# Performance work log

Measured on AMD Instinct MI355X. Metric: run time of the kernel, lower is better.

## Reference

```python
import jax, jax.numpy as jnp
import numpy as np

N_GENE = 4762
N_CELL = 847


def _graph_conv(x_src, src, dst, n_src, n_dst, W, b):
    """DGL GraphConv with norm='both': D_src^{-1/2} A D_dst^{-1/2} X W + b."""
    ones_e = jnp.ones(src.shape, jnp.float32)
    deg_out = jax.ops.segment_sum(ones_e, src, num_segments=n_src)
    norm_src = jnp.clip(deg_out, 1.0, None) ** -0.5
    feat = x_src * norm_src[:, None]            # [n_src, d]
    msg = feat[src]                              # gather  [E, d]
    agg = jax.ops.segment_sum(msg, dst, num_segments=n_dst)  # scatter-add [n_dst, d]
    deg_in = jax.ops.segment_sum(ones_e, dst, num_segments=n_dst)
    norm_dst = jnp.clip(deg_in, 1.0, None) ** -0.5
    return (agg * norm_dst[:, None]) @ W + b


def setup_inputs() -> dict:
    key = jax.random.key(0)
    ks = jax.random.split(key, 12)
    E = 200000
    d = 256
    inp = {
        "gene_emb": jax.random.normal(ks[0], (N_GENE, d), jnp.float32),
        "cell_emb": jax.random.normal(ks[1], (N_CELL, d), jnp.float32),
        "W_g2c": jax.random.normal(ks[2], (d, d), jnp.float32) * (1.0 / np.sqrt(d)),
        "b_g2c": jnp.zeros((d,), jnp.float32),
        "W_c2g": jax.random.normal(ks[3], (d, d), jnp.float32) * (1.0 / np.sqrt(d)),
        "b_c2g": jnp.zeros((d,), jnp.float32),
        "Wp": jax.random.normal(ks[4], (2 * d, 1), jnp.float32) * (1.0 / np.sqrt(2 * d)),
        "bp": jnp.zeros((1,), jnp.float32),
        "g2c_src": jax.random.randint(ks[5], (E,), 0, N_GENE, jnp.int32),
        "g2c_dst": jax.random.randint(ks[6], (E,), 0, N_CELL, jnp.int32),
        "c2g_src": jax.random.randint(ks[7], (E,), 0, N_CELL, jnp.int32),
        "c2g_dst": jax.random.randint(ks[8], (E,), 0, N_GENE, jnp.int32),
        "dec_src": jax.random.randint(ks[9], (E,), 0, N_GENE, jnp.int32),
        "dec_dst": jax.random.randint(ks[10], (E,), 0, N_CELL, jnp.int32),
    }
    return inp


def reference(gene_emb, cell_emb, W_g2c, b_g2c, W_c2g, b_c2g, Wp, bp,
              g2c_src, g2c_dst, c2g_src, c2g_dst, dec_src, dec_dst):
    # HeteroGraphConv (aggregate='sum'): each dst type receives from one relation here.
    h_cell = _graph_conv(gene_emb, g2c_src, g2c_dst, N_GENE, N_CELL, W_g2c, b_g2c)
    h_gene = _graph_conv(cell_emb, c2g_src, c2g_dst, N_CELL, N_GENE, W_c2g, b_c2g)
    h_gene = jax.nn.relu(h_gene)
    h_cell = jax.nn.relu(h_cell)
    # HeteroMLPPredictor: concat(src_h, dst_h) @ Wp + bp on dec_graph edges.
    x = jnp.concatenate([h_gene[dec_src], h_cell[dec_dst]], axis=1)  # [E_dec, 512]
    score = x @ Wp + bp                                               # [E_dec, 1]
    return (score, h_gene, h_cell)
```

## Files before the change

kernel.cpp:

```cpp
#include <hip/hip_runtime.h>

#define N_GENE 4762
#define N_CELL 847
#define NEDGE  200000
#define D      256
#define NPART  64

typedef __attribute__((ext_vector_type(8))) short short8;
typedef __attribute__((ext_vector_type(8))) unsigned short ushort8v;
typedef __attribute__((ext_vector_type(4))) float f32x4;

#define S_G_OUT 0
#define S_C_IN  (S_G_OUT + N_GENE)
#define S_C_OUT (S_C_IN + N_CELL)
#define S_G_IN  (S_C_OUT + N_CELL)
#define NBINS   (S_G_IN + N_GENE)

#define ALIGN8(x) (((x) + 7) & ~7)

#define A_DEG      0
#define A_NRM      (A_DEG + NBINS)
#define A_OFFS_C   (A_NRM + NBINS)
#define A_OFFS_G   (A_OFFS_C + N_CELL + 1)
#define A_SORT_C   ALIGN8(A_OFFS_G + N_GENE + 1)
#define A_SORT_G   (A_SORT_C + 2 * NEDGE)
#define A_PART     (A_SORT_G + 2 * NEDGE)
#define A_SG       (A_PART + NPART * NBINS)
#define A_SC       (A_SG + N_GENE)
#define A_GENE_BF  ALIGN8(A_SC + N_CELL)
#define A_CELL_BF  ALIGN8(A_GENE_BF + N_GENE * D / 2)
#define A_WT1_BF   ALIGN8(A_CELL_BF + N_CELL * D / 2)
#define A_WT2_BF   ALIGN8(A_WT1_BF + D * D / 2)
#define A_AGGC_BF  ALIGN8(A_WT2_BF + D * D / 2)
#define A_AGGG_BF  ALIGN8(A_AGGC_BF + N_CELL * D / 2)

__device__ __forceinline__ unsigned short f2bf(float f) {
    unsigned u = __float_as_uint(f);
    u = (u + 0x7FFFu + ((u >> 16) & 1u)) >> 16;
    return (unsigned short)u;
}
__device__ __forceinline__ float bf2f(unsigned short b) {
    return __uint_as_float(((unsigned)b) << 16);
}

__global__ __launch_bounds__(1024) void k_pre(
        const int* __restrict__ g2c_src, const int* __restrict__ g2c_dst,
        const int* __restrict__ c2g_src, const int* __restrict__ c2g_dst,
        const float* __restrict__ gene_emb, const float* __restrict__ cell_emb,
        const float* __restrict__ W_g2c, const float* __restrict__ W_c2g,
        int* __restrict__ partial,
        unsigned short* __restrict__ gene_bf, unsigned short* __restrict__ cell_bf,
        unsigned short* __restrict__ wt1, unsigned short* __restrict__ wt2) {
    __shared__ int sh[NBINS];
    int B = blockIdx.x, T = threadIdx.x;
    if (B < NPART) {
        for (int j = T; j < NBINS; j += 1024) sh[j] = 0;
        __syncthreads();
        const int chunk = (NEDGE + NPART - 1) / NPART;
        int e0 = B * chunk, e1 = min(NEDGE, e0 + chunk);
        for (int e = e0 + T; e < e1; e += 1024) {
            atomicAdd(&sh[S_G_OUT + g2c_src[e]], 1);
            atomicAdd(&sh[S_C_IN  + g2c_dst[e]], 1);
            atomicAdd(&sh[S_C_OUT + c2g_src[e]], 1);
            atomicAdd(&sh[S_G_IN  + c2g_dst[e]], 1);
        }
        __syncthreads();
        int* pp = partial + B * NBINS;
        for (int j = T; j < NBINS; j += 1024) pp[j] = sh[j];
    } else {
        const int NG = N_GENE * D, NC = N_CELL * D, NW = D * D;
        const int total = NG + NC + 2 * NW;
        for (int i = (B - NPART) * 1024 + T; i < total; i += NPART * 1024) {
            if (i < NG) {
                gene_bf[i] = f2bf(gene_emb[i]);
            } else if (i < NG + NC) {
                int j = i - NG;
                cell_bf[j] = f2bf(cell_emb[j]);
            } else if (i < NG + NC + NW) {
                int j = i - NG - NC;
                wt1[j] = f2bf(W_g2c[(j & 255) * D + (j >> 8)]);
            } else {
                int j = i - NG - NC - NW;
                wt2[j] = f2bf(W_c2g[(j & 255) * D + (j >> 8)]);
            }
        }
    }
}

__global__ void k_reduce(int* __restrict__ partial, int* __restrict__ deg,
                         float* __restrict__ nrm) {
    int j = blockIdx.x * blockDim.x + threadIdx.x;
    if (j < NBINS) {
        int s = 0;
        #pragma unroll
        for (int b0 = 0; b0 < NPART; b0 += 32) {
            int t[32];
            #pragma unroll
            for (int u = 0; u < 32; u++) t[u] = partial[(b0 + u) * NBINS + j];
            #pragma unroll
            for (int u = 0; u < 32; u++) { partial[(b0 + u) * NBINS + j] = s; s += t[u]; }
        }
        deg[j] = s;
        nrm[j] = rsqrtf(fmaxf((float)s, 1.0f));
    }
}

__global__ __launch_bounds__(1024) void k_scatter(
        const int* __restrict__ g2c_src, const int* __restrict__ g2c_dst,
        const int* __restrict__ c2g_src, const int* __restrict__ c2g_dst,
        const int* __restrict__ deg, const int* __restrict__ partial,
        const float* __restrict__ nrm,
        int* __restrict__ offsC, int* __restrict__ offsG,
        int2* __restrict__ sortC, int2* __restrict__ sortG) {
    __shared__ int soffs[N_GENE + 1];
    __shared__ int scur[N_GENE];
    __shared__ int wsum[16];
    int T = threadIdx.x, blk = blockIdx.x, dir = blockIdx.y;
    const int* src  = dir ? c2g_src : g2c_src;
    const int* dst  = dir ? c2g_dst : g2c_dst;
    const int* dgs  = dir ? deg + S_G_IN : deg + S_C_IN;
    const float* nsv = dir ? nrm + S_C_OUT : nrm + S_G_OUT;
    int seg         = dir ? S_G_IN : S_C_IN;
    int nb          = dir ? N_GENE : N_CELL;
    int* goffs      = dir ? offsG : offsC;
    int2* sorted    = dir ? sortG : sortC;
    int per = (nb + 1023) >> 10;
    int i0 = T * per, i1 = min(nb, i0 + per);
    int loc[5];
    int s = 0;
    for (int i = i0; i < i1; i++) { loc[i - i0] = s; s += dgs[i]; }
    int lane = T & 63, w = T >> 6;
    int t = s;
    #pragma unroll
    for (int off = 1; off < 64; off <<= 1) {
        int u = __shfl_up(t, off);
        if (lane >= off) t += u;
    }
    if (lane == 63) wsum[w] = t;
    __syncthreads();
    if (w == 0 && lane < 16) {
        int x = wsum[lane];
        #pragma unroll
        for (int off = 1; off < 16; off <<= 1) {
            int u = __shfl_up(x, off);
            if (lane >= off) x += u;
        }
        wsum[lane] = x;
    }
    __syncthreads();
    int wbase = w ? wsum[w - 1] : 0;
    int excl = wbase + t - s;
    for (int i = i0; i < i1; i++) soffs[i] = excl + loc[i - i0];
    if (T == 1023) soffs[nb] = excl + s;
    __syncthreads();
    if (blk == 0)
        for (int j = T; j <= nb; j += 1024) goffs[j] = soffs[j];
    const int* basep = partial + blk * NBINS + seg;
    for (int j = T; j < nb; j += 1024) scur[j] = soffs[j] + basep[j];
    __syncthreads();
    const int chunk = (NEDGE + NPART - 1) / NPART;
    int e0 = blk * chunk, e1 = min(NEDGE, e0 + chunk);
    for (int e = e0 + T; e < e1; e += 1024) {
        int d = dst[e], sv = src[e];
        float nv = nsv[sv];
        int pos = atomicAdd(&scur[d], 1);
        sorted[pos] = make_int2(sv, __float_as_int(nv));
    }
}

__global__ __launch_bounds__(256) void k_agg(
        const unsigned short* __restrict__ gene_bf,
        const unsigned short* __restrict__ cell_bf,
        const int2* __restrict__ sortC, const int2* __restrict__ sortG,
        const int* __restrict__ offsC, const int* __restrict__ offsG,
        const float* __restrict__ nrm,
        unsigned short* __restrict__ aggC, unsigned short* __restrict__ aggG) {
    __shared__ int   sidx[4][64];
    __shared__ float snrm[4][64];
    __shared__ float pacc[4][256];
    int w = threadIdx.x >> 6, lane = threadIdx.x & 63;
    int half = lane >> 5, li = lane & 31;
    int B = blockIdx.x;
    bool isCell = B < N_CELL;

    int e0, e1;
    const unsigned short* emb;
    const int2* sorted;
    int node;
    if (isCell) {
        node = B;
        int f0 = offsC[node], f1 = offsC[node + 1];
        int ne = f1 - f0, nw = (ne + 3) >> 2;
        e0 = f0 + w * nw; e1 = min(f1, e0 + nw);
        emb = gene_bf; sorted = sortC;
    } else {
        node = (B - N_CELL) * 4 + w;
        if (node >= N_GENE) return;
        e0 = offsG[node]; e1 = offsG[node + 1];
        emb = cell_bf; sorted = sortG;
    }

    float acc[8];
    #pragma unroll
    for (int c = 0; c < 8; c++) acc[c] = 0.f;

    for (int base = e0; base < e1; base += 64) {
        int n = min(64, e1 - base);
        if (lane < n) {
            int2 pr = sorted[base + lane];
            sidx[w][lane] = pr.x;
            snrm[w][lane] = __int_as_float(pr.y);
        }
        int i = 0;
        for (; 2 * i + 8 <= n; i += 4) {
            int j0 = 2 * i + half, j1 = 2 * i + 2 + half;
            int j2 = 2 * i + 4 + half, j3 = 2 * i + 6 + half;
            ushort8v v0 = *(const ushort8v*)&emb[sidx[w][j0] * D + li * 8];
            ushort8v v1 = *(const ushort8v*)&emb[sidx[w][j1] * D + li * 8];
            ushort8v v2 = *(const ushort8v*)&emb[sidx[w][j2] * D + li * 8];
            ushort8v v3 = *(const ushort8v*)&emb[sidx[w][j3] * D + li * 8];
            float n0 = snrm[w][j0], n1 = snrm[w][j1];
            float n2 = snrm[w][j2], n3 = snrm[w][j3];
            #pragma unroll
            for (int c = 0; c < 8; c++)
                acc[c] += bf2f(v0[c]) * n0 + bf2f(v1[c]) * n1 +
                          bf2f(v2[c]) * n2 + bf2f(v3[c]) * n3;
        }
        int npair = (n + 1) >> 1;
        for (; i < npair; i++) {
            int jj = 2 * i + half;
            bool ok = jj < n;
            int idx = ok ? sidx[w][jj] : sidx[w][0];
            float nv = ok ? snrm[w][jj] : 0.f;
            ushort8v v = *(const ushort8v*)&emb[idx * D + li * 8];
            #pragma unroll
            for (int c = 0; c < 8; c++) acc[c] += bf2f(v[c]) * nv;
        }
    }
    #pragma unroll
    for (int c = 0; c < 8; c++) acc[c] += __shfl_xor(acc[c], 32);

    if (isCell) {
        if (half == 0) {
            #pragma unroll
            for (int c = 0; c < 8; c++) pacc[w][li * 8 + c] = acc[c];
        }
        __syncthreads();
        int T = threadIdx.x;
        float s2 = pacc[0][T] + pacc[1][T] + pacc[2][T] + pacc[3][T];
        aggC[node * D + T] = f2bf(s2 * nrm[S_C_IN + node]);
    } else {
        if (half == 0) {
            float ndv = nrm[S_G_IN + node];
            ushort8v o;
            #pragma unroll
            for (int c = 0; c < 8; c++) o[c] = f2bf(acc[c] * ndv);
            *(ushort8v*)&aggG[node * D + li * 8] = o;
        }
    }
}

__global__ __launch_bounds__(256) void k_gemm2(
        const unsigned short* __restrict__ aggC, const unsigned short* __restrict__ aggG,
        const unsigned short* __restrict__ wt1, const unsigned short* __restrict__ wt2,
        const float* __restrict__ b_g2c, const float* __restrict__ b_c2g,
        const float* __restrict__ Wp,
        float* __restrict__ hC, float* __restrict__ hG,
        float* __restrict__ sg, float* __restrict__ sc) {
    const int CT = (N_CELL + 15) / 16;
    const int GT = (N_GENE + 15) / 16;
    int wid = blockIdx.x * 4 + (threadIdx.x >> 6);
    if (wid >= CT + GT) return;
    bool isCell = wid < CT;
    int tile = isCell ? wid : wid - CT;
    int m0 = tile * 16;
    int M = isCell ? N_CELL : N_GENE;
    const unsigned short* A  = isCell ? aggC : aggG;
    const unsigned short* Wt = isCell ? wt1 : wt2;
    const float* bias = isCell ? b_g2c : b_c2g;
    const float* wp   = isCell ? Wp + D : Wp;
    float* H  = isCell ? hC : hG;
    float* sv = isCell ? sc : sg;
    int lane = threadIdx.x & 63;
    int l15 = lane & 15, quad = lane >> 4;
    int arow = m0 + l15;
    if (arow >= M) arow = M - 1;
    f32x4 acc[16];
    #pragma unroll
    for (int t = 0; t < 16; t++) acc[t] = (f32x4){0.f, 0.f, 0.f, 0.f};
    #pragma unroll
    for (int k0 = 0; k0 < D; k0 += 32) {
        short8 a = *(const short8*)&A[arow * D + k0 + quad * 8];
        #pragma unroll
        for (int t = 0; t < 16; t++) {
            short8 b = *(const short8*)&Wt[(t * 16 + l15) * D + k0 + quad * 8];
            acc[t] = __builtin_amdgcn_mfma_f32_16x16x32_bf16(a, b, acc[t], 0, 0, 0);
        }
    }
    float dot[4] = {0.f, 0.f, 0.f, 0.f};
    #pragma unroll
    for (int t = 0; t < 16; t++) {
        int col = t * 16 + l15;
        float bv = bias[col], wv = wp[col];
        #pragma unroll
        for (int r = 0; r < 4; r++) {
            int row = m0 + quad * 4 + r;
            float h = fmaxf(acc[t][r] + bv, 0.f);
            if (row < M) H[row * D + col] = h;
            dot[r] += h * wv;
        }
    }
    #pragma unroll
    for (int off = 1; off < 16; off <<= 1) {
        #pragma unroll
        for (int r = 0; r < 4; r++) dot[r] += __shfl_xor(dot[r], off);
    }
    if (l15 == 0) {
        #pragma unroll
        for (int r = 0; r < 4; r++) {
            int row = m0 + quad * 4 + r;
            if (row < M) sv[row] = dot[r];
        }
    }
}

__global__ void k_score(const int* __restrict__ dsrc, const int* __restrict__ ddst,
                        const float* __restrict__ sg, const float* __restrict__ sc,
                        const float* __restrict__ bp, float* __restrict__ out) {
    int i = blockIdx.x * blockDim.x + threadIdx.x;
    if (i < NEDGE) out[i] = sg[dsrc[i]] + sc[ddst[i]] + bp[0];
}

extern "C" void kernel_launch(void* const* d_in, const int* in_sizes, int n_in,
                              void* d_out, int out_size, void* d_ws, size_t ws_size,
                              hipStream_t stream) {
    const float* gene_emb = (const float*)d_in[0];
    const float* cell_emb = (const float*)d_in[1];
    const float* W_g2c    = (const float*)d_in[2];
    const float* b_g2c    = (const float*)d_in[3];
    const float* W_c2g    = (const float*)d_in[4];
    const float* b_c2g    = (const float*)d_in[5];
    const float* Wp       = (const float*)d_in[6];
    const float* bp       = (const float*)d_in[7];
    const int* g2c_src = (const int*)d_in[8];
    const int* g2c_dst = (const int*)d_in[9];
    const int* c2g_src = (const int*)d_in[10];
    const int* c2g_dst = (const int*)d_in[11];
    const int* dec_src = (const int*)d_in[12];
    const int* dec_dst = (const int*)d_in[13];

    int*   wsi = (int*)d_ws;
    float* wsf = (float*)d_ws;
    unsigned short* gene_bf = (unsigned short*)(wsi + A_GENE_BF);
    unsigned short* cell_bf = (unsigned short*)(wsi + A_CELL_BF);
    unsigned short* wt1     = (unsigned short*)(wsi + A_WT1_BF);
    unsigned short* wt2     = (unsigned short*)(wsi + A_WT2_BF);
    unsigned short* aggC    = (unsigned short*)(wsi + A_AGGC_BF);
    unsigned short* aggG    = (unsigned short*)(wsi + A_AGGG_BF);
    int2* sortC = (int2*)(wsi + A_SORT_C);
    int2* sortG = (int2*)(wsi + A_SORT_G);

    float* out = (float*)d_out;
    float* out_score = out;
    float* out_hgene = out + NEDGE;
    float* out_hcell = out + NEDGE + N_GENE * D;

    k_pre<<<2 * NPART, 1024, 0, stream>>>(g2c_src, g2c_dst, c2g_src, c2g_dst,
                                          gene_emb, cell_emb, W_g2c, W_c2g,
                                          wsi + A_PART, gene_bf, cell_bf, wt1, wt2);
    k_reduce<<<(NBINS + 255) / 256, 256, 0, stream>>>(wsi + A_PART, wsi + A_DEG,
                                                      wsf + A_NRM);
    {
        dim3 grid(NPART, 2);
        k_scatter<<<grid, 1024, 0, stream>>>(g2c_src, g2c_dst, c2g_src, c2g_dst,
                                             wsi + A_DEG, wsi + A_PART, wsf + A_NRM,
                                             wsi + A_OFFS_C, wsi + A_OFFS_G,
                                             sortC, sortG);
    }
    k_agg<<<N_CELL + (N_GENE + 3) / 4, 256, 0, stream>>>(
        gene_bf, cell_bf, sortC, sortG, wsi + A_OFFS_C, wsi + A_OFFS_G,
        wsf + A_NRM, aggC, aggG);
    {
        const int CT = (N_CELL + 15) / 16, GT = (N_GENE + 15) / 16;
        k_gemm2<<<(CT + GT + 3) / 4, 256, 0, stream>>>(aggC, aggG, wt1, wt2,
                                                       b_g2c, b_c2g, Wp,
                                                       out_hcell, out_hgene,
                                                       wsf + A_SG, wsf + A_SC);
    }
    k_score<<<(NEDGE + 255) / 256, 256, 0, stream>>>(dec_src, dec_dst,
                                                     wsf + A_SG, wsf + A_SC, bp, out_score);
}
```

Measured before the change: 158.9 us.

## Fuse front and back kernel chains with software grid barriers; deepen aggregation unroll

```diff
diff --git a/kernel.cpp b/kernel.cpp
--- a/kernel.cpp
+++ b/kernel.cpp
@@ -33,6 +33,7 @@
 #define A_WT2_BF   ALIGN8(A_WT1_BF + D * D / 2)
 #define A_AGGC_BF  ALIGN8(A_WT2_BF + D * D / 2)
 #define A_AGGG_BF  ALIGN8(A_AGGC_BF + N_CELL * D / 2)
+#define A_CTR      ALIGN8(A_AGGG_BF + N_GENE * D / 2)
 
 __device__ __forceinline__ unsigned short f2bf(float f) {
     unsigned u = __float_as_uint(f);
@@ -43,16 +44,37 @@
     return __uint_as_float(((unsigned)b) << 16);
 }
 
-__global__ __launch_bounds__(1024) void k_pre(
+__device__ __forceinline__ void gbar(int* ctr, int target) {
+    __syncthreads();
+    if (threadIdx.x == 0) {
+        __hip_atomic_fetch_add(ctr, 1, __ATOMIC_ACQ_REL, __HIP_MEMORY_SCOPE_AGENT);
+        long long t0 = (long long)__builtin_amdgcn_s_memrealtime();
+        while (__hip_atomic_load(ctr, __ATOMIC_ACQUIRE, __HIP_MEMORY_SCOPE_AGENT) < target) {
+            __builtin_amdgcn_s_sleep(2);
+            if ((long long)__builtin_amdgcn_s_memrealtime() - t0 > 50000000LL) break;
+        }
+    }
+    __syncthreads();
+}
+
+__global__ void k_zero(int* __restrict__ ctrs) {
+    if (threadIdx.x < 4) ctrs[threadIdx.x] = 0;
+}
+
+__global__ __launch_bounds__(1024) void k_front(
         const int* __restrict__ g2c_src, const int* __restrict__ g2c_dst,
         const int* __restrict__ c2g_src, const int* __restrict__ c2g_dst,
         const float* __restrict__ gene_emb, const float* __restrict__ cell_emb,
         const float* __restrict__ W_g2c, const float* __restrict__ W_c2g,
-        int* __restrict__ partial,
+        int* __restrict__ partial, int* __restrict__ deg, float* __restrict__ nrm,
         unsigned short* __restrict__ gene_bf, unsigned short* __restrict__ cell_bf,
-        unsigned short* __restrict__ wt1, unsigned short* __restrict__ wt2) {
+        unsigned short* __restrict__ wt1, unsigned short* __restrict__ wt2,
+        int* __restrict__ offsC, int* __restrict__ offsG,
+        int2* __restrict__ sortC, int2* __restrict__ sortG,
+        int* __restrict__ ctrs) {
     __shared__ int sh[NBINS];
     int B = blockIdx.x, T = threadIdx.x;
+
     if (B < NPART) {
         for (int j = T; j < NBINS; j += 1024) sh[j] = 0;
         __syncthreads();
@@ -85,86 +107,81 @@
             }
         }
     }
-}
-
-__global__ void k_reduce(int* __restrict__ partial, int* __restrict__ deg,
-                         float* __restrict__ nrm) {
-    int j = blockIdx.x * blockDim.x + threadIdx.x;
-    if (j < NBINS) {
+    gbar(&ctrs[0], (int)gridDim.x);
+
+    {
+        int j = B * 1024 + T;
+        if (j < NBINS) {
+            int s = 0;
+            #pragma unroll
+            for (int b0 = 0; b0 < NPART; b0 += 32) {
+                int t[32];
+                #pragma unroll
+                for (int u = 0; u < 32; u++) t[u] = partial[(b0 + u) * NBINS + j];
+                #pragma unroll
+                for (int u = 0; u < 32; u++) { partial[(b0 + u) * NBINS + j] = s; s += t[u]; }
+            }
+            deg[j] = s;
+            nrm[j] = rsqrtf(fmaxf((float)s, 1.0f));
+        }
+    }
+    gbar(&ctrs[1], (int)gridDim.x);
+
+    {
+        int blk = B & (NPART - 1), dir = B >> 6;
+        int* soffs = sh;
+        int* scur  = sh + N_GENE + 1;
+        int* wsum  = sh + 2 * N_GENE + 1;
+        const int* src  = dir ? c2g_src : g2c_src;
+        const int* dst  = dir ? c2g_dst : g2c_dst;
+        const int* dgs  = dir ? deg + S_G_IN : deg + S_C_IN;
+        const float* nsv = dir ? nrm + S_C_OUT : nrm + S_G_OUT;
+        int seg         = dir ? S_G_IN : S_C_IN;
+        int nb          = dir ? N_GENE : N_CELL;
+        int* goffs      = dir ? offsG : offsC;
+        int2* sorted    = dir ? sortG : sortC;
+        int per = (nb + 1023) >> 10;
+        int i0 = T * per, i1 = min(nb, i0 + per);
+        int loc[5];
         int s = 0;
+        for (int i = i0; i < i1; i++) { loc[i - i0] = s; s += dgs[i]; }
+        int lane = T & 63, w = T >> 6;
+        int t = s;
         #pragma unroll
-        for (int b0 = 0; b0 < NPART; b0 += 32) {
-            int t[32];
-            #pragma unroll
-            for (int u = 0; u < 32; u++) t[u] = partial[(b0 + u) * NBINS + j];
-            #pragma unroll
-            for (int u = 0; u < 32; u++) { partial[(b0 + u) * NBINS + j] = s; s += t[u]; }
-        }
-        deg[j] = s;
-        nrm[j] = rsqrtf(fmaxf((float)s, 1.0f));
-    }
-}
-
-__global__ __launch_bounds__(1024) void k_scatter(
-        const int* __restrict__ g2c_src, const int* __restrict__ g2c_dst,
-        const int* __restrict__ c2g_src, const int* __restrict__ c2g_dst,
-        const int* __restrict__ deg, const int* __restrict__ partial,
-        const float* __restrict__ nrm,
-        int* __restrict__ offsC, int* __restrict__ offsG,
-        int2* __restrict__ sortC, int2* __restrict__ sortG) {
-    __shared__ int soffs[N_GENE + 1];
-    __shared__ int scur[N_GENE];
-    __shared__ int wsum[16];
-    int T = threadIdx.x, blk = blockIdx.x, dir = blockIdx.y;
-    const int* src  = dir ? c2g_src : g2c_src;
-    const int* dst  = dir ? c2g_dst : g2c_dst;
-    const int* dgs  = dir ? deg + S_G_IN : deg + S_C_IN;
-    const float* nsv = dir ? nrm + S_C_OUT : nrm + S_G_OUT;
-    int seg         = dir ? S_G_IN : S_C_IN;
-    int nb          = dir ? N_GENE : N_CELL;
-    int* goffs      = dir ? offsG : offsC;
-    int2* sorted    = dir ? sortG : sortC;
-    int per = (nb + 1023) >> 10;
-    int i0 = T * per, i1 = min(nb, i0 + per);
-    int loc[5];
-    int s = 0;
-    for (int i = i0; i < i1; i++) { loc[i - i0] = s; s += dgs[i]; }
-    int lane = T & 63, w = T >> 6;
-    int t = s;
-    #pragma unroll
-    for (int off = 1; off < 64; off <<= 1) {
-        int u = __shfl_up(t, off);
-        if (lane >= off) t += u;
-    }
-    if (lane == 63) wsum[w] = t;
-    __syncthreads();
-    if (w == 0 && lane < 16) {
-        int x = wsum[lane];
-        #pragma unroll
-        for (int off = 1; off < 16; off <<= 1) {
-            int u = __shfl_up(x, off);
-            if (lane >= off) x += u;
-        }
-        wsum[lane] = x;
-    }
-    __syncthreads();
-    int wbase = w ? wsum[w - 1] : 0;
-    int excl = wbase + t - s;
-    for (int i = i0; i < i1; i++) soffs[i] = excl + loc[i - i0];
-    if (T == 1023) soffs[nb] = excl + s;
-    __syncthreads();
-    if (blk == 0)
-        for (int j = T; j <= nb; j += 1024) goffs[j] = soffs[j];
-    const int* basep = partial + blk * NBINS + seg;
-    for (int j = T; j < nb; j += 1024) scur[j] = soffs[j] + basep[j];
-    __syncthreads();
-    const int chunk = (NEDGE + NPART - 1) / NPART;
-    int e0 = blk * chunk, e1 = min(NEDGE, e0 + chunk);
-    for (int e = e0 + T; e < e1; e += 1024) {
-        int d = dst[e], sv = src[e];
-        float nv = nsv[sv];
-        int pos = atomicAdd(&scur[d], 1);
-        sorted[pos] = make_int2(sv, __float_as_int(nv));
+        for (int off = 1; off < 64; off <<= 1) {
+            int u = __shfl_up(t, off);
+            if (lane >= off) t += u;
+        }
+        if (lane == 63) wsum[w] = t;
+        __syncthreads();
+        if (w == 0 && lane < 16) {
+            int x = wsum[lane];
+            #pragma unroll
+            for (int off = 1; off < 16; off <<= 1) {
+                int u = __shfl_up(x, off);
+                if (lane >= off) x += u;
+            }
+            wsum[lane] = x;
+        }
+        __syncthreads();
+        int wbase = w ? wsum[w - 1] : 0;
+        int excl = wbase + t - s;
+        for (int i = i0; i < i1; i++) soffs[i] = excl + loc[i - i0];
+        if (T == 1023) soffs[nb] = excl + s;
+        __syncthreads();
+        if (blk == 0)
+            for (int j = T; j <= nb; j += 1024) goffs[j] = soffs[j];
+        const int* basep = partial + blk * NBINS + seg;
+        for (int j = T; j < nb; j += 1024) scur[j] = soffs[j] + basep[j];
+        __syncthreads();
+        const int chunk = (NEDGE + NPART - 1) / NPART;
+        int e0 = blk * chunk, e1 = min(NEDGE, e0 + chunk);
+        for (int e = e0 + T; e < e1; e += 1024) {
+            int d = dst[e], sv = src[e];
+            float nv = nsv[sv];
+            int pos = atomicAdd(&scur[d], 1);
+            sorted[pos] = make_int2(sv, __float_as_int(nv));
+        }
     }
 }
 
@@ -212,6 +229,23 @@
             snrm[w][lane] = __int_as_float(pr.y);
         }
         int i = 0;
+        for (; 2 * i + 16 <= n; i += 8) {
+            ushort8v v[8];
+            float nv[8];
+            #pragma unroll
+            for (int k = 0; k < 8; k++) {
+                int jj = 2 * i + 2 * k + half;
+                v[k] = *(const ushort8v*)&emb[sidx[w][jj] * D + li * 8];
+                nv[k] = snrm[w][jj];
+            }
+            #pragma unroll
+            for (int c = 0; c < 8; c++) {
+                float s0 = 0.f;
+                #pragma unroll
+                for (int k = 0; k < 8; k++) s0 += bf2f(v[k][c]) * nv[k];
+                acc[c] += s0;
+            }
+        }
         for (; 2 * i + 8 <= n; i += 4) {
             int j0 = 2 * i + half, j1 = 2 * i + 2 + half;
             int j2 = 2 * i + 4 + half, j3 = 2 * i + 6 + half;
@@ -260,75 +294,77 @@
     }
 }
 
-__global__ __launch_bounds__(256) void k_gemm2(
+__global__ __launch_bounds__(256) void k_back(
         const unsigned short* __restrict__ aggC, const unsigned short* __restrict__ aggG,
         const unsigned short* __restrict__ wt1, const unsigned short* __restrict__ wt2,
         const float* __restrict__ b_g2c, const float* __restrict__ b_c2g,
         const float* __restrict__ Wp,
         float* __restrict__ hC, float* __restrict__ hG,
-        float* __restrict__ sg, float* __restrict__ sc) {
+        float* __restrict__ sg, float* __restrict__ sc,
+        const int* __restrict__ dsrc, const int* __restrict__ ddst,
+        const float* __restrict__ bp, float* __restrict__ out,
+        int* __restrict__ ctr) {
     const int CT = (N_CELL + 15) / 16;
     const int GT = (N_GENE + 15) / 16;
     int wid = blockIdx.x * 4 + (threadIdx.x >> 6);
-    if (wid >= CT + GT) return;
-    bool isCell = wid < CT;
-    int tile = isCell ? wid : wid - CT;
-    int m0 = tile * 16;
-    int M = isCell ? N_CELL : N_GENE;
-    const unsigned short* A  = isCell ? aggC : aggG;
-    const unsigned short* Wt = isCell ? wt1 : wt2;
-    const float* bias = isCell ? b_g2c : b_c2g;
-    const float* wp   = isCell ? Wp + D : Wp;
-    float* H  = isCell ? hC : hG;
-    float* sv = isCell ? sc : sg;
-    int lane = threadIdx.x & 63;
-    int l15 = lane & 15, quad = lane >> 4;
-    int arow = m0 + l15;
-    if (arow >= M) arow = M - 1;
-    f32x4 acc[16];
-    #pragma unroll
-    for (int t = 0; t < 16; t++) acc[t] = (f32x4){0.f, 0.f, 0.f, 0.f};
-    #pragma unroll
-    for (int k0 = 0; k0 < D; k0 += 32) {
-        short8 a = *(const short8*)&A[arow * D + k0 + quad * 8];
+    if (wid < CT + GT) {
+        bool isCell = wid < CT;
+        int tile = isCell ? wid : wid - CT;
+        int m0 = tile * 16;
+        int M = isCell ? N_CELL : N_GENE;
+        const unsigned short* A  = isCell ? aggC : aggG;
+        const unsigned short* Wt = isCell ? wt1 : wt2;
+        const float* bias = isCell ? b_g2c : b_c2g;
+        const float* wp   = isCell ? Wp + D : Wp;
+        float* H  = isCell ? hC : hG;
+        float* sv = isCell ? sc : sg;
+        int lane = threadIdx.x & 63;
+        int l15 = lane & 15, quad = lane >> 4;
+        int arow = m0 + l15;
+        if (arow >= M) arow = M - 1;
+        f32x4 acc[16];
+        #pragma unroll
+        for (int t = 0; t < 16; t++) acc[t] = (f32x4){0.f, 0.f, 0.f, 0.f};
+        #pragma unroll
+        for (int k0 = 0; k0 < D; k0 += 32) {
+            short8 a = *(const short8*)&A[arow * D + k0 + quad * 8];
+            #pragma unroll
+            for (int t = 0; t < 16; t++) {
+                short8 b = *(const short8*)&Wt[(t * 16 + l15) * D + k0 + quad * 8];
+                acc[t] = __builtin_amdgcn_mfma_f32_16x16x32_bf16(a, b, acc[t], 0, 0, 0);
+            }
+        }
+        float dot[4] = {0.f, 0.f, 0.f, 0.f};
         #pragma unroll
         for (int t = 0; t < 16; t++) {
-            short8 b = *(const short8*)&Wt[(t * 16 + l15) * D + k0 + quad * 8];
-            acc[t] = __builtin_amdgcn_mfma_f32_16x16x32_bf16(a, b, acc[t], 0, 0, 0);
-        }
-    }
-    float dot[4] = {0.f, 0.f, 0.f, 0.f};
-    #pragma unroll
-    for (int t = 0; t < 16; t++) {
-        int col = t * 16 + l15;
-        float bv = bias[col], wv = wp[col];
+            int col = t * 16 + l15;
+            float bv = bias[col], wv = wp[col];
+            #pragma unroll
+            for (int r = 0; r < 4; r++) {
+                int row = m0 + quad * 4 + r;
+                float h = fmaxf(acc[t][r] + bv, 0.f);
+                if (row < M) H[row * D + col] = h;
+                dot[r] += h * wv;
+            }
+        }
         #pragma unroll
-        for (int r = 0; r < 4; r++) {
-            int row = m0 + quad * 4 + r;
-            float h = fmaxf(acc[t][r] + bv, 0.f);
-            if (row < M) H[row * D + col] = h;
-            dot[r] += h * wv;
-        }
-    }
-    #pragma unroll
-    for (int off = 1; off < 16; off <<= 1) {
-        #pragma unroll
-        for (int r = 0; r < 4; r++) dot[r] += __shfl_xor(dot[r], off);
-    }
-    if (l15 == 0) {
-        #pragma unroll
-        for (int r = 0; r < 4; r++) {
-            int row = m0 + quad * 4 + r;
-            if (row < M) sv[row] = dot[r];
-        }
-    }
-}
-
-__global__ void k_score(const int* __restrict__ dsrc, const int* __restrict__ ddst,
-                        const float* __restrict__ sg, const float* __restrict__ sc,
-                        const float* __restrict__ bp, float* __restrict__ out) {
-    int i = blockIdx.x * blockDim.x + threadIdx.x;
-    if (i < NEDGE) out[i] = sg[dsrc[i]] + sc[ddst[i]] + bp[0];
+        for (int off = 1; off < 16; off <<= 1) {
+            #pragma unroll
+            for (int r = 0; r < 4; r++) dot[r] += __shfl_xor(dot[r], off);
+        }
+        if (l15 == 0) {
+            #pragma unroll
+            for (int r = 0; r < 4; r++) {
+                int row = m0 + quad * 4 + r;
+                if (row < M) sv[row] = dot[r];
+            }
+        }
+    }
+    gbar(ctr, (int)gridDim.x);
+    float bpv = bp[0];
+    int stride = (int)gridDim.x * 256;
+    for (int i = blockIdx.x * 256 + (int)threadIdx.x; i < NEDGE; i += stride)
+        out[i] = sg[dsrc[i]] + sc[ddst[i]] + bpv;
 }
 
 extern "C" void kernel_launch(void* const* d_in, const int* in_sizes, int n_in,
@@ -359,34 +395,23 @@
     unsigned short* aggG    = (unsigned short*)(wsi + A_AGGG_BF);
     int2* sortC = (int2*)(wsi + A_SORT_C);
     int2* sortG = (int2*)(wsi + A_SORT_G);
+    int*  ctrs  = wsi + A_CTR;
 
     float* out = (float*)d_out;
     float* out_score = out;
     float* out_hgene = out + NEDGE;
     float* out_hcell = out + NEDGE + N_GENE * D;
 
-    k_pre<<<2 * NPART, 1024, 0, stream>>>(g2c_src, g2c_dst, c2g_src, c2g_dst,
-                                          gene_emb, cell_emb, W_g2c, W_c2g,
-                                          wsi + A_PART, gene_bf, cell_bf, wt1, wt2);
-    k_reduce<<<(NBINS + 255) / 256, 256, 0, stream>>>(wsi + A_PART, wsi + A_DEG,
-                                                      wsf + A_NRM);
-    {
-        dim3 grid(NPART, 2);
-        k_scatter<<<grid, 1024, 0, stream>>>(g2c_src, g2c_dst, c2g_src, c2g_dst,
-                                             wsi + A_DEG, wsi + A_PART, wsf + A_NRM,
-                                             wsi + A_OFFS_C, wsi + A_OFFS_G,
-                                             sortC, sortG);
-    }
+    k_zero<<<1, 64, 0, stream>>>(ctrs);
+    k_front<<<2 * NPART, 1024, 0, stream>>>(
+        g2c_src, g2c_dst, c2g_src, c2g_dst, gene_emb, cell_emb, W_g2c, W_c2g,
+        wsi + A_PART, wsi + A_DEG, wsf + A_NRM,
+        gene_bf, cell_bf, wt1, wt2,
+        wsi + A_OFFS_C, wsi + A_OFFS_G, sortC, sortG, ctrs);
     k_agg<<<N_CELL + (N_GENE + 3) / 4, 256, 0, stream>>>(
         gene_bf, cell_bf, sortC, sortG, wsi + A_OFFS_C, wsi + A_OFFS_G,
         wsf + A_NRM, aggC, aggG);
-    {
-        const int CT = (N_CELL + 15) / 16, GT = (N_GENE + 15) / 16;
-        k_gemm2<<<(CT + GT + 3) / 4, 256, 0, stream>>>(aggC, aggG, wt1, wt2,
-                                                       b_g2c, b_c2g, Wp,
-                                                       out_hcell, out_hgene,
-                                                       wsf + A_SG, wsf + A_SC);
-    }
-    k_score<<<(NEDGE + 255) / 256, 256, 0, stream>>>(dec_src, dec_dst,
-                                                     wsf + A_SG, wsf + A_SC, bp, out_score);
-}
+    k_back<<<128, 256, 0, stream>>>(aggC, aggG, wt1, wt2, b_g2c, b_c2g, Wp,
+                                    out_hcell, out_hgene, wsf + A_SG, wsf + A_SC,
+                                    dec_src, dec_dst, bp, out_score, ctrs + 2);
+}
```

After: 222.6 us. 40.0% more time.

## Replace sorted sparse aggregation with dense adjacency-count matrix MFMA GEMM

Applied to the files above, without the earlier changes.

```diff
diff --git a/kernel.cpp b/kernel.cpp
--- a/kernel.cpp
+++ b/kernel.cpp
@@ -4,7 +4,8 @@
 #define N_CELL 847
 #define NEDGE  200000
 #define D      256
-#define NPART  64
+#define K1P    4864
+#define K2P    1024
 
 typedef __attribute__((ext_vector_type(8))) short short8;
 typedef __attribute__((ext_vector_type(8))) unsigned short ushort8v;
@@ -18,45 +19,46 @@
 
 #define ALIGN8(x) (((x) + 7) & ~7)
 
-#define A_DEG      0
-#define A_NRM      (A_DEG + NBINS)
-#define A_OFFS_C   (A_NRM + NBINS)
-#define A_OFFS_G   (A_OFFS_C + N_CELL + 1)
-#define A_SORT_C   ALIGN8(A_OFFS_G + N_GENE + 1)
-#define A_SORT_G   (A_SORT_C + 2 * NEDGE)
-#define A_PART     (A_SORT_G + 2 * NEDGE)
-#define A_SG       (A_PART + NPART * NBINS)
-#define A_SC       (A_SG + N_GENE)
-#define A_GENE_BF  ALIGN8(A_SC + N_CELL)
-#define A_CELL_BF  ALIGN8(A_GENE_BF + N_GENE * D / 2)
-#define A_WT1_BF   ALIGN8(A_CELL_BF + N_CELL * D / 2)
-#define A_WT2_BF   ALIGN8(A_WT1_BF + D * D / 2)
-#define A_AGGC_BF  ALIGN8(A_WT2_BF + D * D / 2)
-#define A_AGGG_BF  ALIGN8(A_AGGC_BF + N_CELL * D / 2)
+#define A_DEG   0
+#define A_NRM   (A_DEG + NBINS)
+#define A_SG    (A_NRM + NBINS)
+#define A_SC    (A_SG + N_GENE)
+#define A_WT1   ALIGN8(A_SC + N_CELL)
+#define A_WT2   (A_WT1 + 32768)
+#define A_AGGC  (A_WT2 + 32768)
+#define A_AGGG  (A_AGGC + 108416)
+#define A_FTG   (A_AGGG + 609536)
+#define A_FTC   (A_FTG + 622592)
+#define A_A1    ALIGN8(A_FTC + 131072)
+#define A_A2    (A_A1 + 847 * K1P)
+#define NZERO   (847 * K1P + 4762 * K2P)
 
 __device__ __forceinline__ unsigned short f2bf(float f) {
     unsigned u = __float_as_uint(f);
     u = (u + 0x7FFFu + ((u >> 16) & 1u)) >> 16;
     return (unsigned short)u;
 }
-__device__ __forceinline__ float bf2f(unsigned short b) {
-    return __uint_as_float(((unsigned)b) << 16);
-}
-
-__global__ __launch_bounds__(1024) void k_pre(
+
+__global__ __launch_bounds__(256) void k_z(float* __restrict__ a, int* __restrict__ deg) {
+    const int ZT = NZERO / 4;
+    f32x4 z = {0.f, 0.f, 0.f, 0.f};
+    int gid = blockIdx.x * 256 + threadIdx.x;
+    for (int i = gid; i < ZT; i += 2048 * 256) ((f32x4*)a)[i] = z;
+    if (gid < NBINS) deg[gid] = 0;
+}
+
+__global__ __launch_bounds__(1024) void k_hist(
         const int* __restrict__ g2c_src, const int* __restrict__ g2c_dst,
         const int* __restrict__ c2g_src, const int* __restrict__ c2g_dst,
-        const float* __restrict__ gene_emb, const float* __restrict__ cell_emb,
         const float* __restrict__ W_g2c, const float* __restrict__ W_c2g,
-        int* __restrict__ partial,
-        unsigned short* __restrict__ gene_bf, unsigned short* __restrict__ cell_bf,
+        int* __restrict__ deg, float* __restrict__ A1, float* __restrict__ A2,
         unsigned short* __restrict__ wt1, unsigned short* __restrict__ wt2) {
     __shared__ int sh[NBINS];
     int B = blockIdx.x, T = threadIdx.x;
-    if (B < NPART) {
+    if (B < 64) {
         for (int j = T; j < NBINS; j += 1024) sh[j] = 0;
         __syncthreads();
-        const int chunk = (NEDGE + NPART - 1) / NPART;
+        const int chunk = (NEDGE + 63) / 64;
         int e0 = B * chunk, e1 = min(NEDGE, e0 + chunk);
         for (int e = e0 + T; e < e1; e += 1024) {
             atomicAdd(&sh[S_G_OUT + g2c_src[e]], 1);
@@ -65,198 +67,127 @@
             atomicAdd(&sh[S_G_IN  + c2g_dst[e]], 1);
         }
         __syncthreads();
-        int* pp = partial + B * NBINS;
-        for (int j = T; j < NBINS; j += 1024) pp[j] = sh[j];
+        for (int j = T; j < NBINS; j += 1024) {
+            int v = sh[j];
+            if (v) atomicAdd(&deg[j], v);
+        }
+    } else if (B < 128) {
+        int blk = B - 64;
+        const int chunk = (NEDGE + 63) / 64;
+        int e0 = blk * chunk, e1 = min(NEDGE, e0 + chunk);
+        for (int e = e0 + T; e < e1; e += 1024) {
+            atomicAdd(&A1[g2c_dst[e] * K1P + g2c_src[e]], 1.0f);
+            atomicAdd(&A2[c2g_dst[e] * K2P + c2g_src[e]], 1.0f);
+        }
     } else {
-        const int NG = N_GENE * D, NC = N_CELL * D, NW = D * D;
-        const int total = NG + NC + 2 * NW;
-        for (int i = (B - NPART) * 1024 + T; i < total; i += NPART * 1024) {
-            if (i < NG) {
-                gene_bf[i] = f2bf(gene_emb[i]);
-            } else if (i < NG + NC) {
-                int j = i - NG;
-                cell_bf[j] = f2bf(cell_emb[j]);
-            } else if (i < NG + NC + NW) {
-                int j = i - NG - NC;
-                wt1[j] = f2bf(W_g2c[(j & 255) * D + (j >> 8)]);
+        for (int i = (B - 128) * 1024 + T; i < 2 * 65536; i += 8 * 1024) {
+            if (i < 65536) {
+                wt1[i] = f2bf(W_g2c[(i & 255) * D + (i >> 8)]);
             } else {
-                int j = i - NG - NC - NW;
+                int j = i - 65536;
                 wt2[j] = f2bf(W_c2g[(j & 255) * D + (j >> 8)]);
             }
         }
     }
 }
 
-__global__ void k_reduce(int* __restrict__ partial, int* __restrict__ deg,
-                         float* __restrict__ nrm) {
-    int j = blockIdx.x * blockDim.x + threadIdx.x;
-    if (j < NBINS) {
-        int s = 0;
-        #pragma unroll
-        for (int b0 = 0; b0 < NPART; b0 += 32) {
-            int t[32];
+__global__ void k_nrm(const int* __restrict__ deg, float* __restrict__ nrm) {
+    int j = blockIdx.x * 256 + threadIdx.x;
+    if (j < NBINS) nrm[j] = rsqrtf(fmaxf((float)deg[j], 1.0f));
+}
+
+__global__ __launch_bounds__(256) void k_cvt(
+        const float* __restrict__ gene_emb, const float* __restrict__ cell_emb,
+        const float* __restrict__ nrm,
+        unsigned short* __restrict__ ftg, unsigned short* __restrict__ ftc) {
+    int B = blockIdx.x, T = threadIdx.x;
+    if (B < 256) {
+        int d = B;
+        for (int k0 = T * 8; k0 < K1P; k0 += 2048) {
+            ushort8v o;
             #pragma unroll
-            for (int u = 0; u < 32; u++) t[u] = partial[(b0 + u) * NBINS + j];
+            for (int j = 0; j < 8; j++) {
+                int g = k0 + j;
+                float v = (g < N_GENE) ? gene_emb[g * D + d] * nrm[S_G_OUT + g] : 0.f;
+                o[j] = f2bf(v);
+            }
+            *(ushort8v*)&ftg[d * K1P + k0] = o;
+        }
+    } else {
+        int d = B - 256;
+        for (int k0 = T * 8; k0 < K2P; k0 += 2048) {
+            ushort8v o;
             #pragma unroll
-            for (int u = 0; u < 32; u++) { partial[(b0 + u) * NBINS + j] = s; s += t[u]; }
-        }
-        deg[j] = s;
-        nrm[j] = rsqrtf(fmaxf((float)s, 1.0f));
-    }
-}
-
-__global__ __launch_bounds__(1024) void k_scatter(
-        const int* __restrict__ g2c_src, const int* __restrict__ g2c_dst,
-        const int* __restrict__ c2g_src, const int* __restrict__ c2g_dst,
-        const int* __restrict__ deg, const int* __restrict__ partial,
-        const float* __restrict__ nrm,
-        int* __restrict__ offsC, int* __restrict__ offsG,
-        int2* __restrict__ sortC, int2* __restrict__ sortG) {
-    __shared__ int soffs[N_GENE + 1];
-    __shared__ int scur[N_GENE];
-    __shared__ int wsum[16];
-    int T = threadIdx.x, blk = blockIdx.x, dir = blockIdx.y;
-    const int* src  = dir ? c2g_src : g2c_src;
-    const int* dst  = dir ? c2g_dst : g2c_dst;
-    const int* dgs  = dir ? deg + S_G_IN : deg + S_C_IN;
-    const float* nsv = dir ? nrm + S_C_OUT : nrm + S_G_OUT;
-    int seg         = dir ? S_G_IN : S_C_IN;
-    int nb          = dir ? N_GENE : N_CELL;
-    int* goffs      = dir ? offsG : offsC;
-    int2* sorted    = dir ? sortG : sortC;
-    int per = (nb + 1023) >> 10;
-    int i0 = T * per, i1 = min(nb, i0 + per);
-    int loc[5];
-    int s = 0;
-    for (int i = i0; i < i1; i++) { loc[i - i0] = s; s += dgs[i]; }
-    int lane = T & 63, w = T >> 6;
-    int t = s;
-    #pragma unroll
-    for (int off = 1; off < 64; off <<= 1) {
-        int u = __shfl_up(t, off);
-        if (lane >= off) t += u;
-    }
-    if (lane == 63) wsum[w] = t;
-    __syncthreads();
-    if (w == 0 && lane < 16) {
-        int x = wsum[lane];
-        #pragma unroll
-        for (int off = 1; off < 16; off <<= 1) {
-            int u = __shfl_up(x, off);
-            if (lane >= off) x += u;
-        }
-        wsum[lane] = x;
-    }
-    __syncthreads();
-    int wbase = w ? wsum[w - 1] : 0;
-    int excl = wbase + t - s;
-    for (int i = i0; i < i1; i++) soffs[i] = excl + loc[i - i0];
-    if (T == 1023) soffs[nb] = excl + s;
-    __syncthreads();
-    if (blk == 0)
-        for (int j = T; j <= nb; j += 1024) goffs[j] = soffs[j];
-    const int* basep = partial + blk * NBINS + seg;
-    for (int j = T; j < nb; j += 1024) scur[j] = soffs[j] + basep[j];
-    __syncthreads();
-    const int chunk = (NEDGE + NPART - 1) / NPART;
-    int e0 = blk * chunk, e1 = min(NEDGE, e0 + chunk);
-    for (int e = e0 + T; e < e1; e += 1024) {
-        int d = dst[e], sv = src[e];
-        float nv = nsv[sv];
-        int pos = atomicAdd(&scur[d], 1);
-        sorted[pos] = make_int2(sv, __float_as_int(nv));
-    }
-}
-
-__global__ __launch_bounds__(256) void k_agg(
-        const unsigned short* __restrict__ gene_bf,
-        const unsigned short* __restrict__ cell_bf,
-        const int2* __restrict__ sortC, const int2* __restrict__ sortG,
-        const int* __restrict__ offsC, const int* __restrict__ offsG,
+            for (int j = 0; j < 8; j++) {
+                int c = k0 + j;
+                float v = (c < N_CELL) ? cell_emb[c * D + d] * nrm[S_C_OUT + c] : 0.f;
+                o[j] = f2bf(v);
+            }
+            *(ushort8v*)&ftc[d * K2P + k0] = o;
+        }
+    }
+}
+
+__global__ __launch_bounds__(256) void k_agg_gemm(
+        const float* __restrict__ A1, const float* __restrict__ A2,
+        const unsigned short* __restrict__ ftg, const unsigned short* __restrict__ ftc,
         const float* __restrict__ nrm,
         unsigned short* __restrict__ aggC, unsigned short* __restrict__ aggG) {
-    __shared__ int   sidx[4][64];
-    __shared__ float snrm[4][64];
-    __shared__ float pacc[4][256];
-    int w = threadIdx.x >> 6, lane = threadIdx.x & 63;
-    int half = lane >> 5, li = lane & 31;
-    int B = blockIdx.x;
-    bool isCell = B < N_CELL;
-
-    int e0, e1;
-    const unsigned short* emb;
-    const int2* sorted;
-    int node;
-    if (isCell) {
-        node = B;
-        int f0 = offsC[node], f1 = offsC[node + 1];
-        int ne = f1 - f0, nw = (ne + 3) >> 2;
-        e0 = f0 + w * nw; e1 = min(f1, e0 + nw);
-        emb = gene_bf; sorted = sortC;
-    } else {
-        node = (B - N_CELL) * 4 + w;
-        if (node >= N_GENE) return;
-        e0 = offsG[node]; e1 = offsG[node + 1];
-        emb = cell_bf; sorted = sortG;
-    }
-
-    float acc[8];
-    #pragma unroll
-    for (int c = 0; c < 8; c++) acc[c] = 0.f;
-
-    for (int base = e0; base < e1; base += 64) {
-        int n = min(64, e1 - base);
-        if (lane < n) {
-            int2 pr = sorted[base + lane];
-            sidx[w][lane] = pr.x;
-            snrm[w][lane] = __int_as_float(pr.y);
-        }
-        int i = 0;
-        for (; 2 * i + 8 <= n; i += 4) {
-            int j0 = 2 * i + half, j1 = 2 * i + 2 + half;
-            int j2 = 2 * i + 4 + half, j3 = 2 * i + 6 + half;
-            ushort8v v0 = *(const ushort8v*)&emb[sidx[w][j0] * D + li * 8];
-            ushort8v v1 = *(const ushort8v*)&emb[sidx[w][j1] * D + li * 8];
-            ushort8v v2 = *(const ushort8v*)&emb[sidx[w][j2] * D + li * 8];
-            ushort8v v3 = *(const ushort8v*)&emb[sidx[w][j3] * D + li * 8];
-            float n0 = snrm[w][j0], n1 = snrm[w][j1];
-            float n2 = snrm[w][j2], n3 = snrm[w][j3];
-            #pragma unroll
-            for (int c = 0; c < 8; c++)
-                acc[c] += bf2f(v0[c]) * n0 + bf2f(v1[c]) * n1 +
-                          bf2f(v2[c]) * n2 + bf2f(v3[c]) * n3;
-        }
-        int npair = (n + 1) >> 1;
-        for (; i < npair; i++) {
-            int jj = 2 * i + half;
-            bool ok = jj < n;
-            int idx = ok ? sidx[w][jj] : sidx[w][0];
-            float nv = ok ? snrm[w][jj] : 0.f;
-            ushort8v v = *(const ushort8v*)&emb[idx * D + li * 8];
-            #pragma unroll
-            for (int c = 0; c < 8; c++) acc[c] += bf2f(v[c]) * nv;
-        }
-    }
-    #pragma unroll
-    for (int c = 0; c < 8; c++) acc[c] += __shfl_xor(acc[c], 32);
-
-    if (isCell) {
-        if (half == 0) {
-            #pragma unroll
-            for (int c = 0; c < 8; c++) pacc[w][li * 8 + c] = acc[c];
-        }
-        __syncthreads();
-        int T = threadIdx.x;
-        float s2 = pacc[0][T] + pacc[1][T] + pacc[2][T] + pacc[3][T];
-        aggC[node * D + T] = f2bf(s2 * nrm[S_C_IN + node]);
-    } else {
-        if (half == 0) {
-            float ndv = nrm[S_G_IN + node];
-            ushort8v o;
-            #pragma unroll
-            for (int c = 0; c < 8; c++) o[c] = f2bf(acc[c] * ndv);
-            *(ushort8v*)&aggG[node * D + li * 8] = o;
-        }
+    __shared__ float pacc[16 * 260];
+    const int CT = (N_CELL + 15) / 16;
+    int blk = blockIdx.x, T = threadIdx.x;
+    bool isCell = blk < CT;
+    int tile = isCell ? blk : blk - CT;
+    int m0 = tile * 16;
+    int M  = isCell ? N_CELL : N_GENE;
+    int Kp = isCell ? K1P : K2P;
+    const float* Am = isCell ? A1 : A2;
+    const unsigned short* F = isCell ? ftg : ftc;
+    int nseg = isCell ? S_C_IN : S_G_IN;
+    unsigned short* out = isCell ? aggC : aggG;
+
+    for (int i = T; i < 16 * 260; i += 256) pacc[i] = 0.f;
+    __syncthreads();
+
+    int w = T >> 6, lane = T & 63, l15 = lane & 15, quad = lane >> 4;
+    int arow = m0 + l15;
+    if (arow >= M) arow = M - 1;
+    const float* Ar = Am + arow * Kp;
+    int kspan = Kp >> 2;
+    int kw0 = w * kspan;
+
+    f32x4 acc[16];
+    #pragma unroll
+    for (int t = 0; t < 16; t++) acc[t] = (f32x4){0.f, 0.f, 0.f, 0.f};
+
+    for (int k0 = kw0; k0 < kw0 + kspan; k0 += 32) {
+        const float* ap = Ar + k0 + quad * 8;
+        short8 a;
+        #pragma unroll
+        for (int j = 0; j < 8; j++) a[j] = (short)f2bf(ap[j]);
+        #pragma unroll
+        for (int t = 0; t < 16; t++) {
+            short8 b = *(const short8*)&F[(t * 16 + l15) * Kp + k0 + quad * 8];
+            acc[t] = __builtin_amdgcn_mfma_f32_16x16x32_bf16(a, b, acc[t], 0, 0, 0);
+        }
+    }
+    #pragma unroll
+    for (int t = 0; t < 16; t++)
+        #pragma unroll
+        for (int r = 0; r < 4; r++)
+            atomicAdd(&pacc[(quad * 4 + r) * 260 + t * 16 + l15], acc[t][r]);
+    __syncthreads();
+
+    int row = T >> 4, c0 = (T & 15) * 16;
+    if (m0 + row < M) {
+        float nd = nrm[nseg + m0 + row];
+        ushort8v o;
+        #pragma unroll
+        for (int j = 0; j < 8; j++) o[j] = f2bf(pacc[row * 260 + c0 + j] * nd);
+        *(ushort8v*)&out[(m0 + row) * 256 + c0] = o;
+        #pragma unroll
+        for (int j = 0; j < 8; j++) o[j] = f2bf(pacc[row * 260 + c0 + 8 + j] * nd);
+        *(ushort8v*)&out[(m0 + row) * 256 + c0 + 8] = o;
     }
 }
 
@@ -351,35 +282,30 @@
 
     int*   wsi = (int*)d_ws;
     float* wsf = (float*)d_ws;
-    unsigned short* gene_bf = (unsigned short*)(wsi + A_GENE_BF);
-    unsigned short* cell_bf = (unsigned short*)(wsi + A_CELL_BF);
-    unsigned short* wt1     = (unsigned short*)(wsi + A_WT1_BF);
-    unsigned short* wt2     = (unsigned short*)(wsi + A_WT2_BF);
-    unsigned short* aggC    = (unsigned short*)(wsi + A_AGGC_BF);
-    unsigned short* aggG    = (unsigned short*)(wsi + A_AGGG_BF);
-    int2* sortC = (int2*)(wsi + A_SORT_C);
-    int2* sortG = (int2*)(wsi + A_SORT_G);
+    unsigned short* wt1  = (unsigned short*)(wsi + A_WT1);
+    unsigned short* wt2  = (unsigned short*)(wsi + A_WT2);
+    unsigned short* aggC = (unsigned short*)(wsi + A_AGGC);
+    unsigned short* aggG = (unsigned short*)(wsi + A_AGGG);
+    unsigned short* ftg  = (unsigned short*)(wsi + A_FTG);
+    unsigned short* ftc  = (unsigned short*)(wsi + A_FTC);
+    float* A1 = wsf + A_A1;
+    float* A2 = wsf + A_A2;
 
     float* out = (float*)d_out;
     float* out_score = out;
     float* out_hgene = out + NEDGE;
     float* out_hcell = out + NEDGE + N_GENE * D;
 
-    k_pre<<<2 * NPART, 1024, 0, stream>>>(g2c_src, g2c_dst, c2g_src, c2g_dst,
-                                          gene_emb, cell_emb, W_g2c, W_c2g,
-                                          wsi + A_PART, gene_bf, cell_bf, wt1, wt2);
-    k_reduce<<<(NBINS + 255) / 256, 256, 0, stream>>>(wsi + A_PART, wsi + A_DEG,
-                                                      wsf + A_NRM);
+    k_z<<<2048, 256, 0, stream>>>(A1, wsi + A_DEG);
+    k_hist<<<136, 1024, 0, stream>>>(g2c_src, g2c_dst, c2g_src, c2g_dst,
+                                     W_g2c, W_c2g, wsi + A_DEG, A1, A2, wt1, wt2);
+    k_nrm<<<(NBINS + 255) / 256, 256, 0, stream>>>(wsi + A_DEG, wsf + A_NRM);
+    k_cvt<<<512, 256, 0, stream>>>(gene_emb, cell_emb, wsf + A_NRM, ftg, ftc);
     {
-        dim3 grid(NPART, 2);
-        k_scatter<<<grid, 1024, 0, stream>>>(g2c_src, g2c_dst, c2g_src, c2g_dst,
-                                             wsi + A_DEG, wsi + A_PART, wsf + A_NRM,
-                                             wsi + A_OFFS_C, wsi + A_OFFS_G,
-                                             sortC, sortG);
-    }
-    k_agg<<<N_CELL + (N_GENE + 3) / 4, 256, 0, stream>>>(
-        gene_bf, cell_bf, sortC, sortG, wsi + A_OFFS_C, wsi + A_OFFS_G,
-        wsf + A_NRM, aggC, aggG);
+        const int CT = (N_CELL + 15) / 16, GT = (N_GENE + 15) / 16;
+        k_agg_gemm<<<CT + GT, 256, 0, stream>>>(A1, A2, ftg, ftc, wsf + A_NRM,
+                                                aggC, aggG);
+    }
     {
         const int CT = (N_CELL + 15) / 16, GT = (N_GENE + 15) / 16;
         k_gemm2<<<(CT + GT + 3) / 4, 256, 0, stream>>>(aggC, aggG, wt1, wt2,
```

Measured after the change: 279.7 us. +76.0%, slower.

## Fold degree reduction into scatter kernel and widen aggregation unroll

Applied to the files above, without the earlier changes.

```diff
diff --git a/kernel.cpp b/kernel.cpp
--- a/kernel.cpp
+++ b/kernel.cpp
@@ -18,8 +18,7 @@
 
 #define ALIGN8(x) (((x) + 7) & ~7)
 
-#define A_DEG      0
-#define A_NRM      (A_DEG + NBINS)
+#define A_NRM      0
 #define A_OFFS_C   (A_NRM + NBINS)
 #define A_OFFS_G   (A_OFFS_C + N_CELL + 1)
 #define A_SORT_C   ALIGN8(A_OFFS_G + N_GENE + 1)
@@ -87,48 +86,51 @@
     }
 }
 
-__global__ void k_reduce(int* __restrict__ partial, int* __restrict__ deg,
-                         float* __restrict__ nrm) {
-    int j = blockIdx.x * blockDim.x + threadIdx.x;
-    if (j < NBINS) {
-        int s = 0;
-        #pragma unroll
-        for (int b0 = 0; b0 < NPART; b0 += 32) {
-            int t[32];
-            #pragma unroll
-            for (int u = 0; u < 32; u++) t[u] = partial[(b0 + u) * NBINS + j];
-            #pragma unroll
-            for (int u = 0; u < 32; u++) { partial[(b0 + u) * NBINS + j] = s; s += t[u]; }
-        }
-        deg[j] = s;
-        nrm[j] = rsqrtf(fmaxf((float)s, 1.0f));
-    }
-}
-
 __global__ __launch_bounds__(1024) void k_scatter(
         const int* __restrict__ g2c_src, const int* __restrict__ g2c_dst,
         const int* __restrict__ c2g_src, const int* __restrict__ c2g_dst,
-        const int* __restrict__ deg, const int* __restrict__ partial,
-        const float* __restrict__ nrm,
+        const int* __restrict__ partial, float* __restrict__ nrm,
         int* __restrict__ offsC, int* __restrict__ offsG,
         int2* __restrict__ sortC, int2* __restrict__ sortG) {
-    __shared__ int soffs[N_GENE + 1];
-    __shared__ int scur[N_GENE];
-    __shared__ int wsum[16];
+    __shared__ int   soffs[N_GENE + 1];
+    __shared__ int   scur[N_GENE];
+    __shared__ float nsrcf[N_GENE];
+    __shared__ int   wsum[16];
     int T = threadIdx.x, blk = blockIdx.x, dir = blockIdx.y;
     const int* src  = dir ? c2g_src : g2c_src;
     const int* dst  = dir ? c2g_dst : g2c_dst;
-    const int* dgs  = dir ? deg + S_G_IN : deg + S_C_IN;
-    const float* nsv = dir ? nrm + S_C_OUT : nrm + S_G_OUT;
     int seg         = dir ? S_G_IN : S_C_IN;
+    int sseg        = dir ? S_C_OUT : S_G_OUT;
     int nb          = dir ? N_GENE : N_CELL;
+    int ns          = dir ? N_CELL : N_GENE;
     int* goffs      = dir ? offsG : offsC;
     int2* sorted    = dir ? sortG : sortC;
+
+    for (int j = T; j < ns; j += 1024) {
+        const int* pp = partial + sseg + j;
+        int tot = 0;
+        #pragma unroll 8
+        for (int b = 0; b < NPART; b++) tot += pp[b * NBINS];
+        nsrcf[j] = rsqrtf(fmaxf((float)tot, 1.0f));
+    }
+
     int per = (nb + 1023) >> 10;
     int i0 = T * per, i1 = min(nb, i0 + per);
     int loc[5];
     int s = 0;
-    for (int i = i0; i < i1; i++) { loc[i - i0] = s; s += dgs[i]; }
+    for (int i = i0; i < i1; i++) {
+        const int* pp = partial + seg + i;
+        int tot = 0, rank = 0;
+        #pragma unroll 8
+        for (int b = 0; b < NPART; b++) {
+            int v = pp[b * NBINS];
+            tot += v;
+            if (b < blk) rank += v;
+        }
+        loc[i - i0] = s; s += tot;
+        scur[i] = rank;
+        if (blk == 0) nrm[seg + i] = rsqrtf(fmaxf((float)tot, 1.0f));
+    }
     int lane = T & 63, w = T >> 6;
     int t = s;
     #pragma unroll
@@ -155,14 +157,13 @@
     __syncthreads();
     if (blk == 0)
         for (int j = T; j <= nb; j += 1024) goffs[j] = soffs[j];
-    const int* basep = partial + blk * NBINS + seg;
-    for (int j = T; j < nb; j += 1024) scur[j] = soffs[j] + basep[j];
+    for (int j = T; j < nb; j += 1024) scur[j] += soffs[j];
     __syncthreads();
     const int chunk = (NEDGE + NPART - 1) / NPART;
     int e0 = blk * chunk, e1 = min(NEDGE, e0 + chunk);
     for (int e = e0 + T; e < e1; e += 1024) {
         int d = dst[e], sv = src[e];
-        float nv = nsv[sv];
+        float nv = nsrcf[sv];
         int pos = atomicAdd(&scur[d], 1);
         sorted[pos] = make_int2(sv, __float_as_int(nv));
     }
@@ -212,6 +213,23 @@
             snrm[w][lane] = __int_as_float(pr.y);
         }
         int i = 0;
+        for (; 2 * i + 16 <= n; i += 8) {
+            ushort8v v[8];
+            float nv[8];
+            #pragma unroll
+            for (int k = 0; k < 8; k++) {
+                int jj = 2 * i + 2 * k + half;
+                v[k] = *(const ushort8v*)&emb[sidx[w][jj] * D + li * 8];
+                nv[k] = snrm[w][jj];
+            }
+            #pragma unroll
+            for (int c = 0; c < 8; c++) {
+                float s0 = 0.f;
+                #pragma unroll
+                for (int k = 0; k < 8; k++) s0 += bf2f(v[k][c]) * nv[k];
+                acc[c] += s0;
+            }
+        }
         for (; 2 * i + 8 <= n; i += 4) {
             int j0 = 2 * i + half, j1 = 2 * i + 2 + half;
             int j2 = 2 * i + 4 + half, j3 = 2 * i + 6 + half;
@@ -368,12 +386,10 @@
     k_pre<<<2 * NPART, 1024, 0, stream>>>(g2c_src, g2c_dst, c2g_src, c2g_dst,
                                           gene_emb, cell_emb, W_g2c, W_c2g,
                                           wsi + A_PART, gene_bf, cell_bf, wt1, wt2);
-    k_reduce<<<(NBINS + 255) / 256, 256, 0, stream>>>(wsi + A_PART, wsi + A_DEG,
-                                                      wsf + A_NRM);
     {
         dim3 grid(NPART, 2);
         k_scatter<<<grid, 1024, 0, stream>>>(g2c_src, g2c_dst, c2g_src, c2g_dst,
-                                             wsi + A_DEG, wsi + A_PART, wsf + A_NRM,
+                                             wsi + A_PART, wsf + A_NRM,
                                              wsi + A_OFFS_C, wsi + A_OFFS_G,
                                              sortC, sortG);
     }
```

Measured after the change: 199.4 us. 25.5% more time.
